# Kernel tuning notes

Measured on AMD Instinct MI355X. Metric: run time of the kernel, lower is better.

The kernel has to match this reference:

```python
import jax, jax.numpy as jnp
import numpy as np

B, H, L, D = 4, 16, 2048, 64


def setup_inputs() -> dict:
    key = jax.random.key(0)
    k1, k2, k3 = jax.random.split(key, 3)
    return {
        "query": jax.random.normal(k1, (B, H, L, D), dtype=jnp.float32),
        "key": jax.random.normal(k2, (B, H, L, D), dtype=jnp.float32),
        "value": jax.random.normal(k3, (B, H, D, L), dtype=jnp.float32),
    }


def reference(query, key, value):
    # dot_product_score = Q @ K^T / sqrt(D)   -> [B,H,L,L]
    d = query.shape[-1]
    scores = jnp.einsum("bhqd,bhkd->bhqk", query, key) / jnp.sqrt(jnp.asarray(d, query.dtype))
    attn = jax.nn.softmax(scores, axis=-1)
    # NOTE: original module returns matmul(value, attention_score) = V @ A
    # (value contracted over its last dim L with attn's query dim L) -> [B,H,D,L]
    return jnp.matmul(value, attn)
```

## Files before the change

### kernel.cpp

```cpp
#include <hip/hip_runtime.h>
#include <hip/hip_bf16.h>

#define L_SEQ 2048
#define D_HEAD 64
#define NHEADS 64
#define QSCALE (0.125f * 1.44269504088896340736f)

typedef __attribute__((ext_vector_type(8))) __bf16 bf16x8;
typedef __attribute__((ext_vector_type(16))) float f32x16;

__device__ __forceinline__ int swz(int row, int col) {
    int off = (row << 7) | (col << 1);
    return off ^ ((row & 7) << 4);
}
__device__ __forceinline__ bf16x8 read_frag(const char* lds, int row, int col) {
    return *reinterpret_cast<const bf16x8*>(lds + swz(row, col));
}
__device__ __forceinline__ void pack_write(char* lds, int row, int c4, float4 v,
                                           float4 sc) {
    union { __bf16 h[4]; unsigned long long u; } pk;
    pk.h[0] = (__bf16)(v.x * sc.x);
    pk.h[1] = (__bf16)(v.y * sc.y);
    pk.h[2] = (__bf16)(v.z * sc.z);
    pk.h[3] = (__bf16)(v.w * sc.w);
    *reinterpret_cast<unsigned long long*>(lds + swz(row, c4)) = pk.u;
}

__device__ __forceinline__ int swz128(int row, int col) {
    int off = (row << 8) | (col << 1);
    return off ^ ((row & 15) << 4);
}
__device__ __forceinline__ bf16x8 read_frag128(const char* lds, int row, int col) {
    return *reinterpret_cast<const bf16x8*>(lds + swz128(row, col));
}
__device__ __forceinline__ void pack_write128(char* lds, int row, int c4, float4 v,
                                              float4 sc) {
    union { __bf16 h[4]; unsigned long long u; } pk;
    pk.h[0] = (__bf16)(v.x * sc.x);
    pk.h[1] = (__bf16)(v.y * sc.y);
    pk.h[2] = (__bf16)(v.z * sc.z);
    pk.h[3] = (__bf16)(v.w * sc.w);
    *reinterpret_cast<unsigned long long*>(lds + swz128(row, c4)) = pk.u;
}

__device__ __forceinline__ unsigned cvt_pk_bf16(float lo, float hi) {
    unsigned r;
    asm("v_cvt_pk_bf16_f32 %0, %1, %2" : "=v"(r) : "v"(lo), "v"(hi));
    return r;
}

__global__ __launch_bounds__(256, 4) void attn_pass1(const float* __restrict__ Q,
                                                     const float* __restrict__ K,
                                                     float* __restrict__ invl) {
    __shared__ __align__(16) char lds[16384];
    __shared__ float red[2][128];

    int bid = blockIdx.x;
    int sb = (bid & 7) * 128 + (bid >> 3);
    int bh = sb >> 4;
    int q0 = (sb & 15) << 7;
    const float* Qh = Q + (size_t)bh * L_SEQ * D_HEAD + (size_t)q0 * D_HEAD;
    const float* Kh = K + (size_t)bh * L_SEQ * D_HEAD;

    int t = threadIdx.x, lane = t & 63, w = t >> 6;
    int wq = w >> 1, wk = w & 1;
    int hl = lane >> 5, l31 = lane & 31;
    int r0 = t >> 4;
    int c4 = (t & 15) << 2;

    {
        float4 qs = make_float4(QSCALE, QSCALE, QSCALE, QSCALE);
#pragma unroll
        for (int i = 0; i < 8; ++i) {
            float4 v = *reinterpret_cast<const float4*>(Qh + (size_t)(r0 + i * 16) * D_HEAD + c4);
            pack_write(lds, r0 + i * 16, c4, v, qs);
        }
    }
    __syncthreads();
    bf16x8 qfrag[2][4];
#pragma unroll
    for (int qb = 0; qb < 2; ++qb)
#pragma unroll
        for (int m = 0; m < 4; ++m)
            qfrag[qb][m] = read_frag(lds, wq * 64 + qb * 32 + l31, m * 16 + hl * 8);
    __syncthreads();
    {
        float4 one = make_float4(1.f, 1.f, 1.f, 1.f);
#pragma unroll
        for (int i = 0; i < 4; ++i) {
            float4 v = *reinterpret_cast<const float4*>(Kh + (size_t)(r0 + i * 16) * D_HEAD + c4);
            pack_write(lds, r0 + i * 16, c4, v, one);
        }
    }
    __syncthreads();

    float lsum[2][16];
#pragma unroll
    for (int qb = 0; qb < 2; ++qb)
#pragma unroll
        for (int r = 0; r < 16; ++r) lsum[qb][r] = 0.f;

    for (int k0 = 0; k0 < L_SEQ; k0 += 64) {
        int c = (k0 >> 6) & 1;
        const char* kcur = lds + (c ? 8192 : 0);
        char* knext = lds + (c ? 0 : 8192);

        int nk0 = (k0 + 64) & (L_SEQ - 1);
        float4 kreg[4];
#pragma unroll
        for (int i = 0; i < 4; ++i)
            kreg[i] = *reinterpret_cast<const float4*>(Kh + (size_t)(nk0 + r0 + i * 16) * D_HEAD + c4);

        bf16x8 kfr[4];
#pragma unroll
        for (int m = 0; m < 4; ++m)
            kfr[m] = read_frag(kcur, wk * 32 + l31, m * 16 + hl * 8);

        __builtin_amdgcn_s_setprio(1);
#pragma unroll
        for (int qb = 0; qb < 2; ++qb) {
            f32x16 s;
#pragma unroll
            for (int r = 0; r < 16; ++r) s[r] = 0.f;
#pragma unroll
            for (int m = 0; m < 4; ++m)
                s = __builtin_amdgcn_mfma_f32_32x32x16_bf16(qfrag[qb][m], kfr[m], s, 0, 0, 0);
#pragma unroll
            for (int r = 0; r < 16; ++r)
                lsum[qb][r] += __builtin_amdgcn_exp2f(s[r]);
        }
        __builtin_amdgcn_s_setprio(0);

        {
            float4 one = make_float4(1.f, 1.f, 1.f, 1.f);
#pragma unroll
            for (int i = 0; i < 4; ++i)
                pack_write(knext, r0 + i * 16, c4, kreg[i], one);
        }
        __syncthreads();
    }

#pragma unroll
    for (int qb = 0; qb < 2; ++qb)
#pragma unroll
        for (int r = 0; r < 16; ++r) {
            float v = lsum[qb][r];
            v += __shfl_xor(v, 1);
            v += __shfl_xor(v, 2);
            v += __shfl_xor(v, 4);
            v += __shfl_xor(v, 8);
            v += __shfl_xor(v, 16);
            lsum[qb][r] = v;
        }
    if (l31 == 0) {
#pragma unroll
        for (int qb = 0; qb < 2; ++qb)
#pragma unroll
            for (int r = 0; r < 16; ++r)
                red[wk][wq * 64 + qb * 32 + (r & 3) + 8 * (r >> 2) + 4 * hl] = lsum[qb][r];
    }
    __syncthreads();
    if (t < 128) {
        float ssum = red[0][t] + red[1][t];
        invl[(size_t)bh * L_SEQ + q0 + t] = 1.0f / ssum;
    }
}

__global__ __launch_bounds__(512, 4) void attn_pass2(const float* __restrict__ Q,
                                                     const float* __restrict__ K,
                                                     const float* __restrict__ V,
                                                     const float* __restrict__ invl,
                                                     float* __restrict__ out) {
    __shared__ __align__(16) char lds[65536];

    int bid = blockIdx.x;
    int sb = (bid & 7) * 64 + (bid >> 3);
    int bh = sb >> 3;
    int k0 = (sb & 7) << 8;
    const float* Qh = Q + (size_t)bh * L_SEQ * D_HEAD;
    const float* Kh = K + (size_t)bh * L_SEQ * D_HEAD + (size_t)k0 * D_HEAD;
    const float* Vh = V + (size_t)bh * D_HEAD * L_SEQ;
    const float* il = invl + (size_t)bh * L_SEQ;
    float* Oh = out + (size_t)bh * D_HEAD * L_SEQ;

    int t = threadIdx.x, lane = t & 63, w = t >> 6;
    int hl = lane >> 5, l31 = lane & 31;
    int r0 = t >> 4;
    int c4 = (t & 15) << 2;
    int r0v = t >> 5;
    int c8 = (t & 31) << 2;

    {
        float4 one = make_float4(1.f, 1.f, 1.f, 1.f);
#pragma unroll
        for (int i = 0; i < 8; ++i) {
            float4 v = *reinterpret_cast<const float4*>(Kh + (size_t)(r0 + i * 32) * D_HEAD + c4);
            pack_write(lds, r0 + i * 32, c4, v, one);
        }
    }
    __syncthreads();
    bf16x8 kfrag[4];
#pragma unroll
    for (int m = 0; m < 4; ++m)
        kfrag[m] = read_frag(lds, w * 32 + l31, m * 16 + hl * 8);
    __syncthreads();

    {
        float4 qs = make_float4(QSCALE, QSCALE, QSCALE, QSCALE);
#pragma unroll
        for (int i = 0; i < 4; ++i) {
            float4 v = *reinterpret_cast<const float4*>(Qh + (size_t)(r0 + i * 32) * D_HEAD + c4);
            pack_write(lds, r0 + i * 32, c4, v, qs);
        }
        float4 iv = *reinterpret_cast<const float4*>(il + c8);
#pragma unroll
        for (int i = 0; i < 4; ++i) {
            float4 v = *reinterpret_cast<const float4*>(Vh + (size_t)(r0v + i * 16) * L_SEQ + c8);
            pack_write128(lds + 16384, r0v + i * 16, c8, v, iv);
        }
    }
    __syncthreads();

    f32x16 acc[2];
#pragma unroll
    for (int db = 0; db < 2; ++db)
#pragma unroll
        for (int r = 0; r < 16; ++r) acc[db][r] = 0.f;

    for (int q0 = 0; q0 < L_SEQ; q0 += 128) {
        int c = (q0 >> 7) & 1;
        const char* qcur = lds + (c ? 32768 : 0);
        const char* vcur = qcur + 16384;
        char* qnext = lds + (c ? 0 : 32768);
        char* vnext = qnext + 16384;

        int nq0 = (q0 + 128) & (L_SEQ - 1);
        float4 qreg[4];
#pragma unroll
        for (int i = 0; i < 4; ++i)
            qreg[i] = *reinterpret_cast<const float4*>(Qh + (size_t)(nq0 + r0 + i * 32) * D_HEAD + c4);
        float4 vreg[4], ivn;

#pragma unroll
        for (int qq = 0; qq < 4; ++qq) {
            f32x16 s;
#pragma unroll
            for (int r = 0; r < 16; ++r) s[r] = 0.f;
            __builtin_amdgcn_s_setprio(1);
#pragma unroll
            for (int m = 0; m < 4; ++m) {
                bf16x8 afr = read_frag(qcur, qq * 32 + l31, m * 16 + hl * 8);
                s = __builtin_amdgcn_mfma_f32_32x32x16_bf16(afr, kfrag[m], s, 0, 0, 0);
            }
            __builtin_amdgcn_s_setprio(0);

            unsigned wA[4], wB[4];
#pragma unroll
            for (int g = 0; g < 4; ++g) {
                wA[g] = cvt_pk_bf16(__builtin_amdgcn_exp2f(s[4 * g + 0]),
                                    __builtin_amdgcn_exp2f(s[4 * g + 1]));
                wB[g] = cvt_pk_bf16(__builtin_amdgcn_exp2f(s[4 * g + 2]),
                                    __builtin_amdgcn_exp2f(s[4 * g + 3]));
            }
            bf16x8 pfrag[2];
#pragma unroll
            for (int mm = 0; mm < 2; ++mm) {
                unsigned a0 = wA[2 * mm], b0 = wA[2 * mm + 1];
                unsigned a1 = wB[2 * mm], b1 = wB[2 * mm + 1];
                asm volatile("v_permlane32_swap_b32 %0, %1" : "+v"(a0), "+v"(b0));
                asm volatile("v_permlane32_swap_b32 %0, %1" : "+v"(a1), "+v"(b1));
                union { unsigned u[4]; bf16x8 v; } pk;
                pk.u[0] = a0;
                pk.u[1] = a1;
                pk.u[2] = b0;
                pk.u[3] = b1;
                pfrag[mm] = pk.v;
            }

            __builtin_amdgcn_s_setprio(1);
#pragma unroll
            for (int mm = 0; mm < 2; ++mm)
#pragma unroll
                for (int db = 0; db < 2; ++db) {
                    bf16x8 vfr = read_frag128(vcur, db * 32 + l31, qq * 32 + mm * 16 + hl * 8);
                    acc[db] = __builtin_amdgcn_mfma_f32_32x32x16_bf16(
                        vfr, pfrag[mm], acc[db], 0, 0, 0);
                }
            __builtin_amdgcn_s_setprio(0);

            if (qq == 1) {
                float4 qs = make_float4(QSCALE, QSCALE, QSCALE, QSCALE);
#pragma unroll
                for (int i = 0; i < 4; ++i)
                    pack_write(qnext, r0 + i * 32, c4, qreg[i], qs);
#pragma unroll
                for (int i = 0; i < 4; ++i)
                    vreg[i] = *reinterpret_cast<const float4*>(Vh + (size_t)(r0v + i * 16) * L_SEQ + nq0 + c8);
                ivn = *reinterpret_cast<const float4*>(il + nq0 + c8);
            }
        }
#pragma unroll
        for (int i = 0; i < 4; ++i)
            pack_write128(vnext, r0v + i * 16, c8, vreg[i], ivn);
        __syncthreads();
    }

#pragma unroll
    for (int db = 0; db < 2; ++db)
#pragma unroll
        for (int r = 0; r < 16; ++r) {
            int d = db * 32 + (r & 3) + 8 * (r >> 2) + 4 * hl;
            int k = k0 + w * 32 + l31;
            Oh[(size_t)d * L_SEQ + k] = acc[db][r];
        }
}

extern "C" void kernel_launch(void* const* d_in, const int* in_sizes, int n_in,
                              void* d_out, int out_size, void* d_ws, size_t ws_size,
                              hipStream_t stream) {
    const float* Q = (const float*)d_in[0];
    const float* K = (const float*)d_in[1];
    const float* V = (const float*)d_in[2];
    float* invl = (float*)d_ws;
    float* out = (float*)d_out;

    attn_pass1<<<dim3(NHEADS * (L_SEQ / 128)), dim3(256), 0, stream>>>(Q, K, invl);
    attn_pass2<<<dim3(NHEADS * (L_SEQ / 256)), dim3(512), 0, stream>>>(Q, K, V, invl, out);
}
```

Measured before the change: 139.6 us.

## Restructure both attention passes: per-wave 32-query tiles in pass1, 64-key waves in pass2

```diff
diff --git a/kernel.cpp b/kernel.cpp
--- a/kernel.cpp
+++ b/kernel.cpp
@@ -26,23 +26,6 @@
     *reinterpret_cast<unsigned long long*>(lds + swz(row, c4)) = pk.u;
 }
 
-__device__ __forceinline__ int swz128(int row, int col) {
-    int off = (row << 8) | (col << 1);
-    return off ^ ((row & 15) << 4);
-}
-__device__ __forceinline__ bf16x8 read_frag128(const char* lds, int row, int col) {
-    return *reinterpret_cast<const bf16x8*>(lds + swz128(row, col));
-}
-__device__ __forceinline__ void pack_write128(char* lds, int row, int c4, float4 v,
-                                              float4 sc) {
-    union { __bf16 h[4]; unsigned long long u; } pk;
-    pk.h[0] = (__bf16)(v.x * sc.x);
-    pk.h[1] = (__bf16)(v.y * sc.y);
-    pk.h[2] = (__bf16)(v.z * sc.z);
-    pk.h[3] = (__bf16)(v.w * sc.w);
-    *reinterpret_cast<unsigned long long*>(lds + swz128(row, c4)) = pk.u;
-}
-
 __device__ __forceinline__ unsigned cvt_pk_bf16(float lo, float hi) {
     unsigned r;
     asm("v_cvt_pk_bf16_f32 %0, %1, %2" : "=v"(r) : "v"(lo), "v"(hi));
@@ -52,8 +35,8 @@
 __global__ __launch_bounds__(256, 4) void attn_pass1(const float* __restrict__ Q,
                                                      const float* __restrict__ K,
                                                      float* __restrict__ invl) {
-    __shared__ __align__(16) char lds[16384];
-    __shared__ float red[2][128];
+    __shared__ __align__(16) char lds[32768];
+    __shared__ float red[128];
 
     int bid = blockIdx.x;
     int sb = (bid & 7) * 128 + (bid >> 3);
@@ -63,7 +46,6 @@
     const float* Kh = K + (size_t)bh * L_SEQ * D_HEAD;
 
     int t = threadIdx.x, lane = t & 63, w = t >> 6;
-    int wq = w >> 1, wk = w & 1;
     int hl = lane >> 5, l31 = lane & 31;
     int r0 = t >> 4;
     int c4 = (t & 15) << 2;
@@ -77,96 +59,95 @@
         }
     }
     __syncthreads();
-    bf16x8 qfrag[2][4];
-#pragma unroll
-    for (int qb = 0; qb < 2; ++qb)
-#pragma unroll
-        for (int m = 0; m < 4; ++m)
-            qfrag[qb][m] = read_frag(lds, wq * 64 + qb * 32 + l31, m * 16 + hl * 8);
+    bf16x8 qfrag[4];
+#pragma unroll
+    for (int m = 0; m < 4; ++m)
+        qfrag[m] = read_frag(lds, w * 32 + l31, m * 16 + hl * 8);
     __syncthreads();
     {
         float4 one = make_float4(1.f, 1.f, 1.f, 1.f);
 #pragma unroll
-        for (int i = 0; i < 4; ++i) {
+        for (int i = 0; i < 8; ++i) {
             float4 v = *reinterpret_cast<const float4*>(Kh + (size_t)(r0 + i * 16) * D_HEAD + c4);
             pack_write(lds, r0 + i * 16, c4, v, one);
         }
     }
     __syncthreads();
 
-    float lsum[2][16];
-#pragma unroll
-    for (int qb = 0; qb < 2; ++qb)
-#pragma unroll
-        for (int r = 0; r < 16; ++r) lsum[qb][r] = 0.f;
-
-    for (int k0 = 0; k0 < L_SEQ; k0 += 64) {
-        int c = (k0 >> 6) & 1;
-        const char* kcur = lds + (c ? 8192 : 0);
-        char* knext = lds + (c ? 0 : 8192);
-
-        int nk0 = (k0 + 64) & (L_SEQ - 1);
+    float lsum[16];
+#pragma unroll
+    for (int r = 0; r < 16; ++r) lsum[r] = 0.f;
+
+    for (int k0 = 0; k0 < L_SEQ; k0 += 128) {
+        int c = (k0 >> 7) & 1;
+        const char* kcur = lds + (c ? 16384 : 0);
+        char* knext = lds + (c ? 0 : 16384);
+
+        int nk0 = (k0 + 128) & (L_SEQ - 1);
         float4 kreg[4];
 #pragma unroll
         for (int i = 0; i < 4; ++i)
             kreg[i] = *reinterpret_cast<const float4*>(Kh + (size_t)(nk0 + r0 + i * 16) * D_HEAD + c4);
 
-        bf16x8 kfr[4];
-#pragma unroll
-        for (int m = 0; m < 4; ++m)
-            kfr[m] = read_frag(kcur, wk * 32 + l31, m * 16 + hl * 8);
-
-        __builtin_amdgcn_s_setprio(1);
-#pragma unroll
-        for (int qb = 0; qb < 2; ++qb) {
+#pragma unroll
+        for (int kb = 0; kb < 4; ++kb) {
+            bf16x8 kfr[4];
+#pragma unroll
+            for (int m = 0; m < 4; ++m)
+                kfr[m] = read_frag(kcur, kb * 32 + l31, m * 16 + hl * 8);
+
             f32x16 s;
 #pragma unroll
             for (int r = 0; r < 16; ++r) s[r] = 0.f;
+            __builtin_amdgcn_s_setprio(1);
 #pragma unroll
             for (int m = 0; m < 4; ++m)
-                s = __builtin_amdgcn_mfma_f32_32x32x16_bf16(qfrag[qb][m], kfr[m], s, 0, 0, 0);
+                s = __builtin_amdgcn_mfma_f32_32x32x16_bf16(qfrag[m], kfr[m], s, 0, 0, 0);
+            __builtin_amdgcn_s_setprio(0);
 #pragma unroll
             for (int r = 0; r < 16; ++r)
-                lsum[qb][r] += __builtin_amdgcn_exp2f(s[r]);
-        }
-        __builtin_amdgcn_s_setprio(0);
-
+                lsum[r] += __builtin_amdgcn_exp2f(s[r]);
+
+            if (kb == 1) {
+                float4 one = make_float4(1.f, 1.f, 1.f, 1.f);
+#pragma unroll
+                for (int i = 0; i < 4; ++i)
+                    pack_write(knext, r0 + i * 16, c4, kreg[i], one);
+#pragma unroll
+                for (int i = 0; i < 4; ++i)
+                    kreg[i] = *reinterpret_cast<const float4*>(Kh + (size_t)(nk0 + r0 + (i + 4) * 16) * D_HEAD + c4);
+            }
+        }
         {
             float4 one = make_float4(1.f, 1.f, 1.f, 1.f);
 #pragma unroll
             for (int i = 0; i < 4; ++i)
-                pack_write(knext, r0 + i * 16, c4, kreg[i], one);
+                pack_write(knext, r0 + (i + 4) * 16, c4, kreg[i], one);
         }
         __syncthreads();
     }
 
 #pragma unroll
-    for (int qb = 0; qb < 2; ++qb)
-#pragma unroll
-        for (int r = 0; r < 16; ++r) {
-            float v = lsum[qb][r];
-            v += __shfl_xor(v, 1);
-            v += __shfl_xor(v, 2);
-            v += __shfl_xor(v, 4);
-            v += __shfl_xor(v, 8);
-            v += __shfl_xor(v, 16);
-            lsum[qb][r] = v;
-        }
+    for (int r = 0; r < 16; ++r) {
+        float v = lsum[r];
+        v += __shfl_xor(v, 1);
+        v += __shfl_xor(v, 2);
+        v += __shfl_xor(v, 4);
+        v += __shfl_xor(v, 8);
+        v += __shfl_xor(v, 16);
+        lsum[r] = v;
+    }
     if (l31 == 0) {
 #pragma unroll
-        for (int qb = 0; qb < 2; ++qb)
-#pragma unroll
-            for (int r = 0; r < 16; ++r)
-                red[wk][wq * 64 + qb * 32 + (r & 3) + 8 * (r >> 2) + 4 * hl] = lsum[qb][r];
-    }
-    __syncthreads();
-    if (t < 128) {
-        float ssum = red[0][t] + red[1][t];
-        invl[(size_t)bh * L_SEQ + q0 + t] = 1.0f / ssum;
-    }
-}
-
-__global__ __launch_bounds__(512, 4) void attn_pass2(const float* __restrict__ Q,
+        for (int r = 0; r < 16; ++r)
+            red[w * 32 + (r & 3) + 8 * (r >> 2) + 4 * hl] = lsum[r];
+    }
+    __syncthreads();
+    if (t < 128)
+        invl[(size_t)bh * L_SEQ + q0 + t] = 1.0f / red[t];
+}
+
+__global__ __launch_bounds__(256, 2) void attn_pass2(const float* __restrict__ Q,
                                                      const float* __restrict__ K,
                                                      const float* __restrict__ V,
                                                      const float* __restrict__ invl,
@@ -187,94 +168,106 @@
     int hl = lane >> 5, l31 = lane & 31;
     int r0 = t >> 4;
     int c4 = (t & 15) << 2;
-    int r0v = t >> 5;
-    int c8 = (t & 31) << 2;
 
     {
         float4 one = make_float4(1.f, 1.f, 1.f, 1.f);
 #pragma unroll
-        for (int i = 0; i < 8; ++i) {
-            float4 v = *reinterpret_cast<const float4*>(Kh + (size_t)(r0 + i * 32) * D_HEAD + c4);
-            pack_write(lds, r0 + i * 32, c4, v, one);
-        }
-    }
-    __syncthreads();
-    bf16x8 kfrag[4];
-#pragma unroll
-    for (int m = 0; m < 4; ++m)
-        kfrag[m] = read_frag(lds, w * 32 + l31, m * 16 + hl * 8);
-    __syncthreads();
+        for (int i = 0; i < 16; i += 4) {
+            float4 kr[4];
+#pragma unroll
+            for (int j = 0; j < 4; ++j)
+                kr[j] = *reinterpret_cast<const float4*>(Kh + (size_t)(r0 + (i + j) * 16) * D_HEAD + c4);
+#pragma unroll
+            for (int j = 0; j < 4; ++j)
+                pack_write(lds, r0 + (i + j) * 16, c4, kr[j], one);
+        }
+    }
+    __syncthreads();
+    bf16x8 kfrag[2][4];
+#pragma unroll
+    for (int kb = 0; kb < 2; ++kb)
+#pragma unroll
+        for (int m = 0; m < 4; ++m)
+            kfrag[kb][m] = read_frag(lds, w * 64 + kb * 32 + l31, m * 16 + hl * 8);
 
     {
         float4 qs = make_float4(QSCALE, QSCALE, QSCALE, QSCALE);
+        float4 iv = *reinterpret_cast<const float4*>(il + c4);
 #pragma unroll
         for (int i = 0; i < 4; ++i) {
-            float4 v = *reinterpret_cast<const float4*>(Qh + (size_t)(r0 + i * 32) * D_HEAD + c4);
-            pack_write(lds, r0 + i * 32, c4, v, qs);
-        }
-        float4 iv = *reinterpret_cast<const float4*>(il + c8);
+            float4 qv = *reinterpret_cast<const float4*>(Qh + (size_t)(r0 + i * 16) * D_HEAD + c4);
+            float4 vv = *reinterpret_cast<const float4*>(Vh + (size_t)(r0 + i * 16) * L_SEQ + c4);
+            pack_write(lds + 32768, r0 + i * 16, c4, qv, qs);
+            pack_write(lds + 49152, r0 + i * 16, c4, vv, iv);
+        }
+    }
+    __syncthreads();
+
+    f32x16 acc[2][2];
+#pragma unroll
+    for (int db = 0; db < 2; ++db)
+#pragma unroll
+        for (int kb = 0; kb < 2; ++kb)
+#pragma unroll
+            for (int r = 0; r < 16; ++r) acc[db][kb][r] = 0.f;
+
+    for (int q0 = 0; q0 < L_SEQ; q0 += 64) {
+        int c = (q0 >> 6) & 1;
+        const char* qcur = lds + 32768 + (c ? 8192 : 0);
+        const char* vcur = lds + 49152 + (c ? 8192 : 0);
+        char* qnext = lds + 32768 + (c ? 0 : 8192);
+        char* vnext = lds + 49152 + (c ? 0 : 8192);
+
+        int nq0 = (q0 + 64) & (L_SEQ - 1);
+        float4 qreg[4], vreg[4];
 #pragma unroll
         for (int i = 0; i < 4; ++i) {
-            float4 v = *reinterpret_cast<const float4*>(Vh + (size_t)(r0v + i * 16) * L_SEQ + c8);
-            pack_write128(lds + 16384, r0v + i * 16, c8, v, iv);
-        }
-    }
-    __syncthreads();
-
-    f32x16 acc[2];
-#pragma unroll
-    for (int db = 0; db < 2; ++db)
-#pragma unroll
-        for (int r = 0; r < 16; ++r) acc[db][r] = 0.f;
-
-    for (int q0 = 0; q0 < L_SEQ; q0 += 128) {
-        int c = (q0 >> 7) & 1;
-        const char* qcur = lds + (c ? 32768 : 0);
-        const char* vcur = qcur + 16384;
-        char* qnext = lds + (c ? 0 : 32768);
-        char* vnext = qnext + 16384;
-
-        int nq0 = (q0 + 128) & (L_SEQ - 1);
-        float4 qreg[4];
-#pragma unroll
-        for (int i = 0; i < 4; ++i)
-            qreg[i] = *reinterpret_cast<const float4*>(Qh + (size_t)(nq0 + r0 + i * 32) * D_HEAD + c4);
-        float4 vreg[4], ivn;
-
-#pragma unroll
-        for (int qq = 0; qq < 4; ++qq) {
-            f32x16 s;
-#pragma unroll
-            for (int r = 0; r < 16; ++r) s[r] = 0.f;
+            qreg[i] = *reinterpret_cast<const float4*>(Qh + (size_t)(nq0 + r0 + i * 16) * D_HEAD + c4);
+            vreg[i] = *reinterpret_cast<const float4*>(Vh + (size_t)(r0 + i * 16) * L_SEQ + nq0 + c4);
+        }
+        float4 ivn = *reinterpret_cast<const float4*>(il + nq0 + c4);
+
+#pragma unroll
+        for (int qq = 0; qq < 2; ++qq) {
+            f32x16 s[2];
+#pragma unroll
+            for (int kb = 0; kb < 2; ++kb)
+#pragma unroll
+                for (int r = 0; r < 16; ++r) s[kb][r] = 0.f;
+
             __builtin_amdgcn_s_setprio(1);
 #pragma unroll
             for (int m = 0; m < 4; ++m) {
                 bf16x8 afr = read_frag(qcur, qq * 32 + l31, m * 16 + hl * 8);
-                s = __builtin_amdgcn_mfma_f32_32x32x16_bf16(afr, kfrag[m], s, 0, 0, 0);
+                s[0] = __builtin_amdgcn_mfma_f32_32x32x16_bf16(afr, kfrag[0][m], s[0], 0, 0, 0);
+                s[1] = __builtin_amdgcn_mfma_f32_32x32x16_bf16(afr, kfrag[1][m], s[1], 0, 0, 0);
             }
             __builtin_amdgcn_s_setprio(0);
 
-            unsigned wA[4], wB[4];
-#pragma unroll
-            for (int g = 0; g < 4; ++g) {
-                wA[g] = cvt_pk_bf16(__builtin_amdgcn_exp2f(s[4 * g + 0]),
-                                    __builtin_amdgcn_exp2f(s[4 * g + 1]));
-                wB[g] = cvt_pk_bf16(__builtin_amdgcn_exp2f(s[4 * g + 2]),
-                                    __builtin_amdgcn_exp2f(s[4 * g + 3]));
-            }
-            bf16x8 pfrag[2];
-#pragma unroll
-            for (int mm = 0; mm < 2; ++mm) {
-                unsigned a0 = wA[2 * mm], b0 = wA[2 * mm + 1];
-                unsigned a1 = wB[2 * mm], b1 = wB[2 * mm + 1];
-                asm volatile("v_permlane32_swap_b32 %0, %1" : "+v"(a0), "+v"(b0));
-                asm volatile("v_permlane32_swap_b32 %0, %1" : "+v"(a1), "+v"(b1));
-                union { unsigned u[4]; bf16x8 v; } pk;
-                pk.u[0] = a0;
-                pk.u[1] = a1;
-                pk.u[2] = b0;
-                pk.u[3] = b1;
-                pfrag[mm] = pk.v;
+            bf16x8 pfrag[2][2];
+#pragma unroll
+            for (int kb = 0; kb < 2; ++kb) {
+                unsigned wA[4], wB[4];
+#pragma unroll
+                for (int g = 0; g < 4; ++g) {
+                    wA[g] = cvt_pk_bf16(__builtin_amdgcn_exp2f(s[kb][4 * g + 0]),
+                                        __builtin_amdgcn_exp2f(s[kb][4 * g + 1]));
+                    wB[g] = cvt_pk_bf16(__builtin_amdgcn_exp2f(s[kb][4 * g + 2]),
+                                        __builtin_amdgcn_exp2f(s[kb][4 * g + 3]));
+                }
+#pragma unroll
+                for (int mm = 0; mm < 2; ++mm) {
+                    unsigned a0 = wA[2 * mm], b0 = wA[2 * mm + 1];
+                    unsigned a1 = wB[2 * mm], b1 = wB[2 * mm + 1];
+                    asm volatile("v_permlane32_swap_b32 %0, %1" : "+v"(a0), "+v"(b0));
+                    asm volatile("v_permlane32_swap_b32 %0, %1" : "+v"(a1), "+v"(b1));
+                    union { unsigned u[4]; bf16x8 v; } pk;
+                    pk.u[0] = a0;
+                    pk.u[1] = a1;
+                    pk.u[2] = b0;
+                    pk.u[3] = b1;
+                    pfrag[kb][mm] = pk.v;
+                }
             }
 
             __builtin_amdgcn_s_setprio(1);
@@ -282,37 +275,36 @@
             for (int mm = 0; mm < 2; ++mm)
 #pragma unroll
                 for (int db = 0; db < 2; ++db) {
-                    bf16x8 vfr = read_frag128(vcur, db * 32 + l31, qq * 32 + mm * 16 + hl * 8);
-                    acc[db] = __builtin_amdgcn_mfma_f32_32x32x16_bf16(
-                        vfr, pfrag[mm], acc[db], 0, 0, 0);
+                    bf16x8 vfr = read_frag(vcur, db * 32 + l31, qq * 32 + mm * 16 + hl * 8);
+#pragma unroll
+                    for (int kb = 0; kb < 2; ++kb)
+                        acc[db][kb] = __builtin_amdgcn_mfma_f32_32x32x16_bf16(
+                            vfr, pfrag[kb][mm], acc[db][kb], 0, 0, 0);
                 }
             __builtin_amdgcn_s_setprio(0);
-
-            if (qq == 1) {
-                float4 qs = make_float4(QSCALE, QSCALE, QSCALE, QSCALE);
-#pragma unroll
-                for (int i = 0; i < 4; ++i)
-                    pack_write(qnext, r0 + i * 32, c4, qreg[i], qs);
-#pragma unroll
-                for (int i = 0; i < 4; ++i)
-                    vreg[i] = *reinterpret_cast<const float4*>(Vh + (size_t)(r0v + i * 16) * L_SEQ + nq0 + c8);
-                ivn = *reinterpret_cast<const float4*>(il + nq0 + c8);
-            }
-        }
-#pragma unroll
-        for (int i = 0; i < 4; ++i)
-            pack_write128(vnext, r0v + i * 16, c8, vreg[i], ivn);
+        }
+
+        {
+            float4 qs = make_float4(QSCALE, QSCALE, QSCALE, QSCALE);
+#pragma unroll
+            for (int i = 0; i < 4; ++i) {
+                pack_write(qnext, r0 + i * 16, c4, qreg[i], qs);
+                pack_write(vnext, r0 + i * 16, c4, vreg[i], ivn);
+            }
+        }
         __syncthreads();
     }
 
 #pragma unroll
     for (int db = 0; db < 2; ++db)
 #pragma unroll
-        for (int r = 0; r < 16; ++r) {
-            int d = db * 32 + (r & 3) + 8 * (r >> 2) + 4 * hl;
-            int k = k0 + w * 32 + l31;
-            Oh[(size_t)d * L_SEQ + k] = acc[db][r];
-        }
+        for (int kb = 0; kb < 2; ++kb)
+#pragma unroll
+            for (int r = 0; r < 16; ++r) {
+                int d = db * 32 + (r & 3) + 8 * (r >> 2) + 4 * hl;
+                int k = k0 + w * 64 + kb * 32 + l31;
+                Oh[(size_t)d * L_SEQ + k] = acc[db][kb][r];
+            }
 }
 
 extern "C" void kernel_launch(void* const* d_in, const int* in_sizes, int n_in,
@@ -325,5 +317,5 @@
     float* out = (float*)d_out;
 
     attn_pass1<<<dim3(NHEADS * (L_SEQ / 128)), dim3(256), 0, stream>>>(Q, K, invl);
-    attn_pass2<<<dim3(NHEADS * (L_SEQ / 256)), dim3(512), 0, stream>>>(Q, K, V, invl, out);
-}
+    attn_pass2<<<dim3(NHEADS * (L_SEQ / 256)), dim3(256), 0, stream>>>(Q, K, V, invl, out);
+}
```

After: 199.4 us. 1.43x slower.

## Split pass2 warps across query halves with 64-key tiles and LDS reduction

Applied to the files above, without the earlier changes.

```diff
diff --git a/kernel.cpp b/kernel.cpp
--- a/kernel.cpp
+++ b/kernel.cpp
@@ -184,25 +184,25 @@
     float* Oh = out + (size_t)bh * D_HEAD * L_SEQ;
 
     int t = threadIdx.x, lane = t & 63, w = t >> 6;
+    int wq = w >> 2, wk = w & 3;
     int hl = lane >> 5, l31 = lane & 31;
     int r0 = t >> 4;
     int c4 = (t & 15) << 2;
     int r0v = t >> 5;
     int c8 = (t & 31) << 2;
 
-    {
-        float4 one = make_float4(1.f, 1.f, 1.f, 1.f);
-#pragma unroll
-        for (int i = 0; i < 8; ++i) {
-            float4 v = *reinterpret_cast<const float4*>(Kh + (size_t)(r0 + i * 32) * D_HEAD + c4);
-            pack_write(lds, r0 + i * 32, c4, v, one);
-        }
-    }
-    __syncthreads();
-    bf16x8 kfrag[4];
-#pragma unroll
-    for (int m = 0; m < 4; ++m)
-        kfrag[m] = read_frag(lds, w * 32 + l31, m * 16 + hl * 8);
+#pragma unroll
+    for (int i = 0; i < 8; ++i) {
+        float4 v = *reinterpret_cast<const float4*>(Kh + (size_t)(r0 + i * 32) * D_HEAD + c4);
+        pack_write(lds, r0 + i * 32, c4, v, make_float4(1.f, 1.f, 1.f, 1.f));
+    }
+    __syncthreads();
+    bf16x8 kfrag[2][4];
+#pragma unroll
+    for (int kb = 0; kb < 2; ++kb)
+#pragma unroll
+        for (int m = 0; m < 4; ++m)
+            kfrag[kb][m] = read_frag(lds, wk * 64 + kb * 32 + l31, m * 16 + hl * 8);
     __syncthreads();
 
     {
@@ -221,11 +221,13 @@
     }
     __syncthreads();
 
-    f32x16 acc[2];
+    f32x16 acc[2][2];
 #pragma unroll
     for (int db = 0; db < 2; ++db)
 #pragma unroll
-        for (int r = 0; r < 16; ++r) acc[db][r] = 0.f;
+        for (int kb = 0; kb < 2; ++kb)
+#pragma unroll
+            for (int r = 0; r < 16; ++r) acc[db][kb][r] = 0.f;
 
     for (int q0 = 0; q0 < L_SEQ; q0 += 128) {
         int c = (q0 >> 7) & 1;
@@ -235,84 +237,112 @@
         char* vnext = qnext + 16384;
 
         int nq0 = (q0 + 128) & (L_SEQ - 1);
-        float4 qreg[4];
+        float4 qreg[4], vreg[4];
 #pragma unroll
         for (int i = 0; i < 4; ++i)
             qreg[i] = *reinterpret_cast<const float4*>(Qh + (size_t)(nq0 + r0 + i * 32) * D_HEAD + c4);
-        float4 vreg[4], ivn;
-
-#pragma unroll
-        for (int qq = 0; qq < 4; ++qq) {
-            f32x16 s;
-#pragma unroll
-            for (int r = 0; r < 16; ++r) s[r] = 0.f;
+#pragma unroll
+        for (int i = 0; i < 4; ++i)
+            vreg[i] = *reinterpret_cast<const float4*>(Vh + (size_t)(r0v + i * 16) * L_SEQ + nq0 + c8);
+        float4 ivn = *reinterpret_cast<const float4*>(il + nq0 + c8);
+
+#pragma unroll
+        for (int qq = 0; qq < 2; ++qq) {
+            int qrow = (wq * 2 + qq) * 32;
+
+            f32x16 s[2];
+#pragma unroll
+            for (int kb = 0; kb < 2; ++kb)
+#pragma unroll
+                for (int r = 0; r < 16; ++r) s[kb][r] = 0.f;
+
             __builtin_amdgcn_s_setprio(1);
 #pragma unroll
             for (int m = 0; m < 4; ++m) {
-                bf16x8 afr = read_frag(qcur, qq * 32 + l31, m * 16 + hl * 8);
-                s = __builtin_amdgcn_mfma_f32_32x32x16_bf16(afr, kfrag[m], s, 0, 0, 0);
+                bf16x8 afr = read_frag(qcur, qrow + l31, m * 16 + hl * 8);
+                s[0] = __builtin_amdgcn_mfma_f32_32x32x16_bf16(afr, kfrag[0][m], s[0], 0, 0, 0);
+                s[1] = __builtin_amdgcn_mfma_f32_32x32x16_bf16(afr, kfrag[1][m], s[1], 0, 0, 0);
             }
             __builtin_amdgcn_s_setprio(0);
 
-            unsigned wA[4], wB[4];
-#pragma unroll
-            for (int g = 0; g < 4; ++g) {
-                wA[g] = cvt_pk_bf16(__builtin_amdgcn_exp2f(s[4 * g + 0]),
-                                    __builtin_amdgcn_exp2f(s[4 * g + 1]));
-                wB[g] = cvt_pk_bf16(__builtin_amdgcn_exp2f(s[4 * g + 2]),
-                                    __builtin_amdgcn_exp2f(s[4 * g + 3]));
+            bf16x8 pfrag[2][2];
+#pragma unroll
+            for (int kb = 0; kb < 2; ++kb) {
+                unsigned wA[4], wB[4];
+#pragma unroll
+                for (int g = 0; g < 4; ++g) {
+                    wA[g] = cvt_pk_bf16(__builtin_amdgcn_exp2f(s[kb][4 * g + 0]),
+                                        __builtin_amdgcn_exp2f(s[kb][4 * g + 1]));
+                    wB[g] = cvt_pk_bf16(__builtin_amdgcn_exp2f(s[kb][4 * g + 2]),
+                                        __builtin_amdgcn_exp2f(s[kb][4 * g + 3]));
+                }
+#pragma unroll
+                for (int mm = 0; mm < 2; ++mm) {
+                    unsigned a0 = wA[2 * mm], b0 = wA[2 * mm + 1];
+                    unsigned a1 = wB[2 * mm], b1 = wB[2 * mm + 1];
+                    asm volatile("v_permlane32_swap_b32 %0, %1" : "+v"(a0), "+v"(b0));
+                    asm volatile("v_permlane32_swap_b32 %0, %1" : "+v"(a1), "+v"(b1));
+                    union { unsigned u[4]; bf16x8 v; } pk;
+                    pk.u[0] = a0;
+                    pk.u[1] = a1;
+                    pk.u[2] = b0;
+                    pk.u[3] = b1;
+                    pfrag[kb][mm] = pk.v;
+                }
             }
-            bf16x8 pfrag[2];
-#pragma unroll
-            for (int mm = 0; mm < 2; ++mm) {
-                unsigned a0 = wA[2 * mm], b0 = wA[2 * mm + 1];
-                unsigned a1 = wB[2 * mm], b1 = wB[2 * mm + 1];
-                asm volatile("v_permlane32_swap_b32 %0, %1" : "+v"(a0), "+v"(b0));
-                asm volatile("v_permlane32_swap_b32 %0, %1" : "+v"(a1), "+v"(b1));
-                union { unsigned u[4]; bf16x8 v; } pk;
-                pk.u[0] = a0;
-                pk.u[1] = a1;
-                pk.u[2] = b0;
-                pk.u[3] = b1;
-                pfrag[mm] = pk.v;
-            }
 
             __builtin_amdgcn_s_setprio(1);
 #pragma unroll
             for (int mm = 0; mm < 2; ++mm)
 #pragma unroll
                 for (int db = 0; db < 2; ++db) {
-                    bf16x8 vfr = read_frag128(vcur, db * 32 + l31, qq * 32 + mm * 16 + hl * 8);
-                    acc[db] = __builtin_amdgcn_mfma_f32_32x32x16_bf16(
-                        vfr, pfrag[mm], acc[db], 0, 0, 0);
+                    bf16x8 vfr = read_frag128(vcur, db * 32 + l31, qrow + mm * 16 + hl * 8);
+#pragma unroll
+                    for (int kb = 0; kb < 2; ++kb)
+                        acc[db][kb] = __builtin_amdgcn_mfma_f32_32x32x16_bf16(
+                            vfr, pfrag[kb][mm], acc[db][kb], 0, 0, 0);
                 }
             __builtin_amdgcn_s_setprio(0);
-
-            if (qq == 1) {
-                float4 qs = make_float4(QSCALE, QSCALE, QSCALE, QSCALE);
-#pragma unroll
-                for (int i = 0; i < 4; ++i)
-                    pack_write(qnext, r0 + i * 32, c4, qreg[i], qs);
-#pragma unroll
-                for (int i = 0; i < 4; ++i)
-                    vreg[i] = *reinterpret_cast<const float4*>(Vh + (size_t)(r0v + i * 16) * L_SEQ + nq0 + c8);
-                ivn = *reinterpret_cast<const float4*>(il + nq0 + c8);
-            }
-        }
-#pragma unroll
-        for (int i = 0; i < 4; ++i)
-            pack_write128(vnext, r0v + i * 16, c8, vreg[i], ivn);
+        }
+
+        {
+            float4 qs = make_float4(QSCALE, QSCALE, QSCALE, QSCALE);
+#pragma unroll
+            for (int i = 0; i < 4; ++i)
+                pack_write(qnext, r0 + i * 32, c4, qreg[i], qs);
+#pragma unroll
+            for (int i = 0; i < 4; ++i)
+                pack_write128(vnext, r0v + i * 16, c8, vreg[i], ivn);
+        }
         __syncthreads();
     }
 
-#pragma unroll
-    for (int db = 0; db < 2; ++db)
-#pragma unroll
-        for (int r = 0; r < 16; ++r) {
-            int d = db * 32 + (r & 3) + 8 * (r >> 2) + 4 * hl;
-            int k = k0 + w * 32 + l31;
-            Oh[(size_t)d * L_SEQ + k] = acc[db][r];
-        }
+    __syncthreads();
+    float* exf = reinterpret_cast<float*>(lds);
+    if (wq == 1) {
+#pragma unroll
+        for (int db = 0; db < 2; ++db)
+#pragma unroll
+            for (int kb = 0; kb < 2; ++kb)
+#pragma unroll
+                for (int r = 0; r < 16; ++r)
+                    exf[(((wk * 2 + db) * 2 + kb) * 16 + r) * 64 + lane] = acc[db][kb][r];
+    }
+    __syncthreads();
+    if (wq == 0) {
+#pragma unroll
+        for (int db = 0; db < 2; ++db)
+#pragma unroll
+            for (int kb = 0; kb < 2; ++kb)
+#pragma unroll
+                for (int r = 0; r < 16; ++r) {
+                    float v = acc[db][kb][r] +
+                              exf[(((wk * 2 + db) * 2 + kb) * 16 + r) * 64 + lane];
+                    int d = db * 32 + (r & 3) + 8 * (r >> 2) + 4 * hl;
+                    int k = k0 + wk * 64 + kb * 32 + l31;
+                    Oh[(size_t)d * L_SEQ + k] = v;
+                }
+    }
 }
 
 extern "C" void kernel_launch(void* const* d_in, const int* in_sizes, int n_in,
```

After: 287.8 us. +106.1%, slower.
